# Kernel optimization log

Hardware: AMD Instinct MI355X
Metric: run time of the kernel (lower is better)

Reference implementation:

```python
import math
import jax, jax.numpy as jnp
import numpy as np

# module constants (mirror __init__ with m=5, n=2, groups=4, dilation=2)
M = 5                       # Taylor order param
N = 2
U = 1 + 2 ** (N - 1)        # unit_FZ = 3
GROUPS = 4
DIL = 2                     # self.dilation
BOUNDARY = math.sqrt(math.ceil((M - 1) / 2))  # sqrt(2)
KSIZE = U * (M - 1) + 1     # 13


def _pad_to(t, T):
    """pad_num: center-pad last dim up to length T (extra on the right if odd)."""
    d = T - t.shape[-1]
    return jnp.pad(t, [(0, 0), (0, 0), (d // 2, d - d // 2)])


def setup_inputs() -> dict:
    key = jax.random.key(0)
    k1, k2, k3 = jax.random.split(key, 3)
    B, C, T = 8, 256, 16384
    O = 256
    fan_in = (C // GROUPS) * KSIZE
    x = jax.random.normal(k1, (B, C, T), dtype=jnp.float32)
    w = jax.random.normal(k2, (O, C // GROUPS, KSIZE), dtype=jnp.float32) / math.sqrt(fan_in)
    b = jax.random.normal(k3, (O,), dtype=jnp.float32) / math.sqrt(fan_in)
    return {"x": x, "w": w, "b": b}


def reference(x, w, b):
    B, C, T = x.shape
    O = w.shape[0]
    out = jnp.zeros((B, O, T), dtype=x.dtype)
    for i in range(DIL):
        xs = x[:, :, i::DIL]                      # (B, C, Ti)
        Ti = xs.shape[-1]
        # zero-insertion (stride-U upsample) fused into the conv via lhs_dilation,
        # grouped conv1d with padding U-1 on both sides
        y = jax.lax.conv_general_dilated(
            xs, w, window_strides=(1,), padding=[(U - 1, U - 1)],
            lhs_dilation=(U,), rhs_dilation=(1,),
            dimension_numbers=("NCH", "OIH", "NCH"),
            feature_group_count=GROUPS,
        ) + b[None, :, None]                      # (B, O, Lout)
        lst = []
        # j == 0: base term + detached neighbor-difference denominator
        t0 = _pad_to(y[:, :, U - 1::U], Ti)       # (B, O, Ti)
        lst.append(t0)
        t0d = jax.lax.stop_gradient(t0)
        pl = (M - 1) // 2
        pr = (M - 1) - pl
        padded = jnp.pad(t0d, [(0, 0), (0, 0), (pl, pr)])
        # windows[b,c,k,t] = padded[b,c,t+k]  (size-M time neighborhood)
        win = jnp.stack([padded[:, :, k:k + Ti] for k in range(M)], axis=2)  # (B,O,M,Ti)
        denom = jnp.clip((t0d[:, :, None, :] - win).mean(axis=2), 1.0, BOUNDARY)
        # j >= 1: strided finite differences
        for j in range(1, U):
            d = y[:, :, j - 1 + U::U] - y[:, :, :-U][:, :, j - 1::U]
            lst.append(_pad_to(d, Ti) / denom)
        # recursive log2-depth higher-order combination
        if len(lst) > 2:
            n_order = math.floor(math.log2(len(lst) - 1)) + 1
            ro = 2
            while ro <= n_order:
                cal = lst[-2 ** (n_order - ro + 1):]
                for k in range(2 ** (n_order - ro)):
                    xk = cal[2 ** (n_order - ro) + k] - cal[2 ** (n_order - ro) - k - 1]
                    xk = xk / (2 ** (n_order - ro))
                    lst.append(_pad_to(math.factorial(ro) * xk, Ti) / denom)
                ro += 1
        dia = jnp.mean(jnp.stack(lst, axis=0), axis=0)  # (B, O, Ti)
        out = out.at[:, :, i::DIL].set(dia)
    return out
```

## Files before the change

kernel.cpp:

```cpp
#include <hip/hip_runtime.h>


typedef float v4f __attribute__((ext_vector_type(4)));
typedef short v8s __attribute__((ext_vector_type(8)));

#define TI 8192
#define TFULL 16384
#define TB 64
#define XPH_BYTES 10752
#define T0L_F 0
#define D2L_F 5440
#define D1L_F 10880
#define BIAS_F 16320
#define LDS_BYTES 65536

__device__ __forceinline__ unsigned bf16w(float f) {
    unsigned u = __float_as_uint(f);
    return (u + 0x7FFFu + ((u >> 16) & 1u)) >> 16;
}

__global__ void prep_kernel(const float* __restrict__ w, unsigned short* __restrict__ gw) {
    int id = blockIdx.x * 256 + threadIdx.x;
    int j    = id & 7;
    int lane = (id >> 3) & 63;
    int fid  = id >> 9;
    int mt   = fid % 12;  fid /= 12;
    int kc   = fid & 1;   fid >>= 1;
    int e    = fid % 5;
    int g    = fid / 5;
    int a  = mt >> 2;
    int mg = mt & 3;
    int o  = 16 * mg + (lane & 15);
    int c  = 32 * kc + (lane >> 4) * 8 + j;
    const float* wb = w + (((size_t)(g * 64 + o)) * 64 + c) * 13;
    float val;
    if (a == 0) {
        val = wb[3 * e];
    } else {
        int tap = (a == 1) ? 1 : 2;
        float lo = (e > 0) ? wb[3 * (e - 1) + tap] : 0.0f;
        float hi = (e < 4) ? wb[3 * e + tap] : 0.0f;
        val = lo - hi;
    }
    gw[id] = (unsigned short)bf16w(val);
}

__global__ __launch_bounds__(512, 4)
void pconv_mfma(const unsigned short* __restrict__ gw, const float* __restrict__ x,
                const float* __restrict__ bias, float* __restrict__ out) {
    extern __shared__ char smem[];
    float* smemf = (float*)smem;

    const int tid  = threadIdx.x;
    const int lane = tid & 63;
    const int wv   = tid >> 6;
    const int mg   = wv >> 1;
    const int ph   = wv & 1;
    const int col  = lane & 15;
    const int quad = lane >> 4;

    const int tileIdx = blockIdx.x;
    const int g       = blockIdx.y;
    const int b       = blockIdx.z;
    const int tb      = tileIdx * TB;

    if (tid < 64) smemf[BIAS_F + tid] = bias[g * 64 + tid];

    {
        const float* xb = x + ((size_t)(b * 256 + g * 64)) * TFULL;
        const int v0 = 2 * tb - 8;
        for (int f = tid; f < 1344; f += 512) {
            int q  = f % 42;
            int cp = f / 42;
            int vq = v0 + 4 * q;
            const float* r0 = xb + (size_t)(2 * cp) * TFULL;
            const float* r1 = r0 + TFULL;
            float a0, a1, a2, a3, b0, b1, b2, b3;
            if (vq >= 0 && vq + 3 < TFULL) {
                v4f A4 = *(const v4f*)(r0 + vq);
                v4f B4 = *(const v4f*)(r1 + vq);
                a0 = A4[0]; a1 = A4[1]; a2 = A4[2]; a3 = A4[3];
                b0 = B4[0]; b1 = B4[1]; b2 = B4[2]; b3 = B4[3];
            } else {
                a0 = (vq >= 0 && vq < TFULL) ? r0[vq] : 0.0f;
                a1 = (vq + 1 >= 0 && vq + 1 < TFULL) ? r0[vq + 1] : 0.0f;
                a2 = (vq + 2 >= 0 && vq + 2 < TFULL) ? r0[vq + 2] : 0.0f;
                a3 = (vq + 3 >= 0 && vq + 3 < TFULL) ? r0[vq + 3] : 0.0f;
                b0 = (vq >= 0 && vq < TFULL) ? r1[vq] : 0.0f;
                b1 = (vq + 1 >= 0 && vq + 1 < TFULL) ? r1[vq + 1] : 0.0f;
                b2 = (vq + 2 >= 0 && vq + 2 < TFULL) ? r1[vq + 2] : 0.0f;
                b3 = (vq + 3 >= 0 && vq + 3 < TFULL) ? r1[vq + 3] : 0.0f;
            }
            int cblk = cp >> 2;
            int woff = (cp & 3) * 4;
            unsigned w0 = bf16w(a0) | (bf16w(b0) << 16);
            unsigned w1 = bf16w(a1) | (bf16w(b1) << 16);
            unsigned w2 = bf16w(a2) | (bf16w(b2) << 16);
            unsigned w3 = bf16w(a3) | (bf16w(b3) << 16);
            int t0r = 2 * q, t1r = 2 * q + 1;
            *(unsigned*)(smem + 0 * XPH_BYTES + t0r * 128 + ((cblk ^ (t0r & 7)) << 4) + woff) = w0;
            *(unsigned*)(smem + 1 * XPH_BYTES + t0r * 128 + ((cblk ^ (t0r & 7)) << 4) + woff) = w1;
            *(unsigned*)(smem + 0 * XPH_BYTES + t1r * 128 + ((cblk ^ (t1r & 7)) << 4) + woff) = w2;
            *(unsigned*)(smem + 1 * XPH_BYTES + t1r * 128 + ((cblk ^ (t1r & 7)) << 4) + woff) = w3;
        }
    }
    __syncthreads();

    const unsigned short* gwp = gw + (size_t)g * 61440;
    v4f acc[3][5];
    #pragma unroll
    for (int a = 0; a < 3; ++a)
        #pragma unroll
        for (int u = 0; u < 5; ++u) acc[a][u] = (v4f){0.f, 0.f, 0.f, 0.f};

    const char* xph = smem + ph * XPH_BYTES;
    #pragma unroll
    for (int e = 0; e < 5; ++e) {
        #pragma unroll
        for (int kc = 0; kc < 2; ++kc) {
            v8s Af[3];
            #pragma unroll
            for (int a = 0; a < 3; ++a)
                Af[a] = *(const v8s*)(gwp + (((e * 2 + kc) * 12 + 4 * a + mg) << 9) + (lane << 3));
            const int sw = (col + e) * 128 + (((4 * kc + quad) ^ ((col + e) & 7)) << 4);
            #pragma unroll
            for (int u = 0; u < 5; ++u) {
                v8s Bf = *(const v8s*)(xph + u * 2048 + sw);
                #pragma unroll
                for (int a = 0; a < 3; ++a)
                    acc[a][u] = __builtin_amdgcn_mfma_f32_16x16x32_bf16(Af[a], Bf, acc[a][u], 0, 0, 0);
            }
        }
    }
    __syncthreads();

    const int o0 = 16 * mg + 4 * quad;
    const v4f bias4 = *(const v4f*)(smemf + BIAS_F + o0);
    const size_t outbase = ((size_t)(b * 256 + g * 64)) * TFULL;

    #pragma unroll
    for (int p = 0; p < 2; ++p) {
        if (ph == p) {
            #pragma unroll
            for (int a = 0; a < 3; ++a) {
                float* dst = smemf + (a == 0 ? T0L_F : (a == 1 ? D2L_F : D1L_F));
                #pragma unroll
                for (int u = 0; u < 5; ++u) {
                    int idx = 16 * u + col;
                    int t = tb - 2 + idx;
                    bool valid = (t >= 2) && (t <= TI - 3);
                    v4f v = acc[a][u];
                    if (a == 0) v = v + bias4;
                    if (!valid) v = (v4f){0.f, 0.f, 0.f, 0.f};
                    *(v4f*)(dst + idx * 68 + o0) = v;
                }
            }
        }
        __syncthreads();
        #pragma unroll
        for (int it = 0; it < 2; ++it) {
            int f = tid + it * 512;
            int jq = f & 15;
            int o  = f >> 4;
            float* ob = out + outbase + (size_t)o * TFULL;
            #pragma unroll
            for (int s = 0; s < 4; ++s) {
                int j = jq + 16 * s;
                float w0 = smemf[T0L_F + (j + 0) * 68 + o];
                float w1 = smemf[T0L_F + (j + 1) * 68 + o];
                float w2 = smemf[T0L_F + (j + 2) * 68 + o];
                float w3 = smemf[T0L_F + (j + 3) * 68 + o];
                float w4 = smemf[T0L_F + (j + 4) * 68 + o];
                float d2v = smemf[D2L_F + (j + 2) * 68 + o];
                float d1v = smemf[D1L_F + (j + 2) * 68 + o];
                float t0 = w2;
                float m5 = 0.2f * (w0 + w1 + w2 + w3 + w4);
                float den = fminf(fmaxf(t0 - m5, 1.0f), 1.41421356237309515f);
                float rc = 1.0f / den;
                float res = 0.25f * (t0 + (d1v + d2v) * rc +
                                     2.0f * (d2v - d1v) * rc * rc);
                ob[2 * (tb + j) + p] = res;
            }
        }
        __syncthreads();
    }
}

extern "C" void kernel_launch(void* const* d_in, const int* in_sizes, int n_in,
                              void* d_out, int out_size, void* d_ws, size_t ws_size,
                              hipStream_t stream) {
    const float* x  = (const float*)d_in[0];
    const float* w  = (const float*)d_in[1];
    const float* bb = (const float*)d_in[2];
    float* out = (float*)d_out;

    unsigned short* gw = (unsigned short*)d_ws;

    prep_kernel<<<960, 256, 0, stream>>>(w, gw);
    pconv_mfma<<<dim3(128, 4, 8), 512, LDS_BYTES, stream>>>(gw, x, bb, out);
}
```

Baseline: 308.0 us.

## Compute epilogue in registers via swapped MFMA operands and lane shuffles

Swaps the MFMA A/B operands so each lane holds consecutive time samples for a single output channel. The 5-point neighborhood mean can then be formed with cross-lane shuffles instead of staging three result tiles through LDS. This removes the LDS epilogue buffers, the two-phase loop and its barriers, and shrinks LDS use from 64KB to 21KB, which may allow more resident blocks. Input conversion also switches to the packed bf16 intrinsic. The tradeoff is that output stores become strided and less coalesced, and the shuffles add some work.

After: 335.6 us. 8.9% more time.

```diff
diff --git a/kernel.cpp b/kernel.cpp
--- a/kernel.cpp
+++ b/kernel.cpp
@@ -1,4 +1,5 @@
 #include <hip/hip_runtime.h>
+#include <hip/hip_bf16.h>
 
 
 typedef float v4f __attribute__((ext_vector_type(4)));
@@ -8,15 +9,17 @@
 #define TFULL 16384
 #define TB 64
 #define XPH_BYTES 10752
-#define T0L_F 0
-#define D2L_F 5440
-#define D1L_F 10880
-#define BIAS_F 16320
-#define LDS_BYTES 65536
+#define LDS_BYTES 21504
 
 __device__ __forceinline__ unsigned bf16w(float f) {
     unsigned u = __float_as_uint(f);
     return (u + 0x7FFFu + ((u >> 16) & 1u)) >> 16;
+}
+
+__device__ __forceinline__ unsigned packbf2(float lo, float hi) {
+    union { __hip_bfloat162 h; unsigned u; } cv;
+    cv.h = __float22bfloat162_rn(make_float2(lo, hi));
+    return cv.u;
 }
 
 __global__ void prep_kernel(const float* __restrict__ w, unsigned short* __restrict__ gw) {
@@ -49,7 +52,6 @@
 void pconv_mfma(const unsigned short* __restrict__ gw, const float* __restrict__ x,
                 const float* __restrict__ bias, float* __restrict__ out) {
     extern __shared__ char smem[];
-    float* smemf = (float*)smem;
 
     const int tid  = threadIdx.x;
     const int lane = tid & 63;
@@ -63,8 +65,6 @@
     const int g       = blockIdx.y;
     const int b       = blockIdx.z;
     const int tb      = tileIdx * TB;
-
-    if (tid < 64) smemf[BIAS_F + tid] = bias[g * 64 + tid];
 
     {
         const float* xb = x + ((size_t)(b * 256 + g * 64)) * TFULL;
@@ -93,10 +93,10 @@
             }
             int cblk = cp >> 2;
             int woff = (cp & 3) * 4;
-            unsigned w0 = bf16w(a0) | (bf16w(b0) << 16);
-            unsigned w1 = bf16w(a1) | (bf16w(b1) << 16);
-            unsigned w2 = bf16w(a2) | (bf16w(b2) << 16);
-            unsigned w3 = bf16w(a3) | (bf16w(b3) << 16);
+            unsigned w0 = packbf2(a0, b0);
+            unsigned w1 = packbf2(a1, b1);
+            unsigned w2 = packbf2(a2, b2);
+            unsigned w3 = packbf2(a3, b3);
             int t0r = 2 * q, t1r = 2 * q + 1;
             *(unsigned*)(smem + 0 * XPH_BYTES + t0r * 128 + ((cblk ^ (t0r & 7)) << 4) + woff) = w0;
             *(unsigned*)(smem + 1 * XPH_BYTES + t0r * 128 + ((cblk ^ (t0r & 7)) << 4) + woff) = w1;
@@ -128,61 +128,70 @@
                 v8s Bf = *(const v8s*)(xph + u * 2048 + sw);
                 #pragma unroll
                 for (int a = 0; a < 3; ++a)
-                    acc[a][u] = __builtin_amdgcn_mfma_f32_16x16x32_bf16(Af[a], Bf, acc[a][u], 0, 0, 0);
-            }
-        }
-    }
-    __syncthreads();
-
-    const int o0 = 16 * mg + 4 * quad;
-    const v4f bias4 = *(const v4f*)(smemf + BIAS_F + o0);
-    const size_t outbase = ((size_t)(b * 256 + g * 64)) * TFULL;
-
-    #pragma unroll
-    for (int p = 0; p < 2; ++p) {
-        if (ph == p) {
+                    acc[a][u] = __builtin_amdgcn_mfma_f32_16x16x32_bf16(Bf, Af[a], acc[a][u], 0, 0, 0);
+            }
+        }
+    }
+
+    const int oG = g * 64 + 16 * mg + col;
+    const float bias_s = bias[oG];
+    float* ob = out + ((size_t)(b * 256 + oG)) * TFULL;
+    const bool edge = (tileIdx == 0) || (tileIdx == 127);
+
+    #pragma unroll
+    for (int u = 0; u < 5; ++u) {
+        v4f t0v = acc[0][u];
+        #pragma unroll
+        for (int r = 0; r < 4; ++r) t0v[r] += bias_s;
+        if (edge) {
+            v4f d2v = acc[1][u];
+            v4f d1v = acc[2][u];
             #pragma unroll
-            for (int a = 0; a < 3; ++a) {
-                float* dst = smemf + (a == 0 ? T0L_F : (a == 1 ? D2L_F : D1L_F));
-                #pragma unroll
-                for (int u = 0; u < 5; ++u) {
-                    int idx = 16 * u + col;
-                    int t = tb - 2 + idx;
-                    bool valid = (t >= 2) && (t <= TI - 3);
-                    v4f v = acc[a][u];
-                    if (a == 0) v = v + bias4;
-                    if (!valid) v = (v4f){0.f, 0.f, 0.f, 0.f};
-                    *(v4f*)(dst + idx * 68 + o0) = v;
-                }
-            }
-        }
-        __syncthreads();
-        #pragma unroll
-        for (int it = 0; it < 2; ++it) {
-            int f = tid + it * 512;
-            int jq = f & 15;
-            int o  = f >> 4;
-            float* ob = out + outbase + (size_t)o * TFULL;
-            #pragma unroll
-            for (int s = 0; s < 4; ++s) {
-                int j = jq + 16 * s;
-                float w0 = smemf[T0L_F + (j + 0) * 68 + o];
-                float w1 = smemf[T0L_F + (j + 1) * 68 + o];
-                float w2 = smemf[T0L_F + (j + 2) * 68 + o];
-                float w3 = smemf[T0L_F + (j + 3) * 68 + o];
-                float w4 = smemf[T0L_F + (j + 4) * 68 + o];
-                float d2v = smemf[D2L_F + (j + 2) * 68 + o];
-                float d1v = smemf[D1L_F + (j + 2) * 68 + o];
-                float t0 = w2;
-                float m5 = 0.2f * (w0 + w1 + w2 + w3 + w4);
-                float den = fminf(fmaxf(t0 - m5, 1.0f), 1.41421356237309515f);
-                float rc = 1.0f / den;
-                float res = 0.25f * (t0 + (d1v + d2v) * rc +
-                                     2.0f * (d2v - d1v) * rc * rc);
-                ob[2 * (tb + j) + p] = res;
-            }
-        }
-        __syncthreads();
+            for (int r = 0; r < 4; ++r) {
+                int t = tb - 2 + 16 * u + 4 * quad + r;
+                if (t < 2 || t > TI - 3) { t0v[r] = 0.f; d2v[r] = 0.f; d1v[r] = 0.f; }
+            }
+            acc[1][u] = d2v;
+            acc[2][u] = d1v;
+        }
+        acc[0][u] = t0v;
+    }
+
+    const int tlb = (lane + 48) & 63;
+    const int tla = (lane + 16) & 63;
+    #pragma unroll
+    for (int u = 0; u < 5; ++u) {
+        const v4f Tm = acc[0][u];
+        const v4f Tp = acc[0][u > 0 ? u - 1 : 0];
+        const v4f Tn = acc[0][u < 4 ? u + 1 : 4];
+        float b2o = __shfl(Tm[2], tlb), b2s = __shfl(Tp[2], tlb);
+        float b1o = __shfl(Tm[3], tlb), b1s = __shfl(Tp[3], tlb);
+        float a0o = __shfl(Tm[0], tla), a0s = __shfl(Tn[0], tla);
+        float a1o = __shfl(Tm[1], tla), a1s = __shfl(Tn[1], tla);
+        float wn[8];
+        wn[0] = (quad == 0) ? b2s : b2o;
+        wn[1] = (quad == 0) ? b1s : b1o;
+        wn[2] = Tm[0]; wn[3] = Tm[1]; wn[4] = Tm[2]; wn[5] = Tm[3];
+        wn[6] = (quad == 3) ? a0s : a0o;
+        wn[7] = (quad == 3) ? a1s : a1o;
+        #pragma unroll
+        for (int r = 0; r < 4; ++r) {
+            float t0 = wn[r + 2];
+            float m5 = 0.2f * (wn[r] + wn[r + 1] + wn[r + 2] + wn[r + 3] + wn[r + 4]);
+            float den = fminf(fmaxf(t0 - m5, 1.0f), 1.41421356237309515f);
+            float rc = 1.0f / den;
+            float d2 = acc[1][u][r];
+            float d1 = acc[2][u][r];
+            float res = 0.25f * (t0 + (d1 + d2) * rc + 2.0f * (d2 - d1) * rc * rc);
+            int j = 16 * u + 4 * quad + r - 2;
+            if (u == 0) {
+                if (j >= 0) ob[2 * (tb + j) + ph] = res;
+            } else if (u == 4) {
+                if (j < TB) ob[2 * (tb + j) + ph] = res;
+            } else {
+                ob[2 * (tb + j) + ph] = res;
+            }
+        }
     }
 }
 
```
